# Kernel optimization log

Measured on AMD Instinct MI355X. Metric: run time of the kernel, lower is better.

## Reference

```python
import jax, jax.numpy as jnp
import numpy as np

N_NODES = 4096
F_UAV = 64
N_OBS = N_NODES * F_UAV + 256  # 262400
H = 1024
N_ACT = 64
N_EDGES = 65536


def setup_inputs() -> dict:
    key = jax.random.key(0)
    ks = jax.random.split(key, 13)
    s = lambda fan_in: 1.0 / np.sqrt(fan_in)
    return {
        "node_x": jax.random.normal(ks[0], (N_NODES, F_UAV), jnp.float32),
        "flat_obs": jax.random.normal(ks[1], (N_OBS,), jnp.float32),
        "gcn_w": jax.random.normal(ks[2], (F_UAV, F_UAV), jnp.float32) * s(F_UAV),
        "gcn_b": jnp.zeros((F_UAV,), jnp.float32),
        "w1": jax.random.normal(ks[3], (N_OBS, H), jnp.float32) * s(N_OBS),
        "b1": jnp.zeros((H,), jnp.float32),
        "w2": jax.random.normal(ks[4], (H, H), jnp.float32) * s(H),
        "b2": jnp.zeros((H,), jnp.float32),
        "wv": jax.random.normal(ks[5], (H, 1), jnp.float32) * s(H),
        "bv": jnp.zeros((1,), jnp.float32),
        "wa": jax.random.normal(ks[6], (H, N_ACT), jnp.float32) * s(H),
        "ba": jnp.zeros((N_ACT,), jnp.float32),
        "edge_index": jax.random.randint(ks[7], (2, N_EDGES), 0, N_NODES, jnp.int64),
    }


def _gcn_conv(x, edge_index, w, b):
    n = x.shape[0]
    loops = jnp.arange(n, dtype=edge_index.dtype)
    src = jnp.concatenate([edge_index[0], loops])
    dst = jnp.concatenate([edge_index[1], loops])
    deg = jax.ops.segment_sum(jnp.ones_like(dst, dtype=x.dtype), dst, num_segments=n)
    dinv = jax.lax.rsqrt(deg)  # deg >= 1 thanks to self-loops
    norm = dinv[src] * dinv[dst]          # [E+N]
    h = x @ w                              # [N, F]
    msg = h[src] * norm[:, None]           # gather + scale
    out = jax.ops.segment_sum(msg, dst, num_segments=n)  # scatter-add
    return out + b


def reference(node_x, flat_obs, gcn_w, gcn_b, w1, b1, w2, b2, wv, bv, wa, ba, edge_index):
    y_uav = _gcn_conv(node_x, edge_index, gcn_w, gcn_b).reshape(-1)  # flatten
    x = jnp.concatenate([y_uav, flat_obs[y_uav.shape[0]:]], axis=0)  # [N_OBS]
    y = jax.nn.relu(x @ w1 + b1)
    y = jax.nn.relu(y @ w2 + b2)
    value = y @ wv + bv                    # [1]
    adv = y @ wa + ba                      # [N_ACT]
    return value + adv - jnp.mean(adv, keepdims=True)
```

## Files before the change

kernel.cpp:

```cpp
#include <hip/hip_runtime.h>

#define N_NODES 4096
#define F_UAV 64
#define NOBS 262400
#define GCN_FLAT (N_NODES * F_UAV)
#define HDIM 1024
#define N_ACT 64
#define N_EDGES 65536

typedef float f32x4 __attribute__((ext_vector_type(4)));
typedef float f32x2 __attribute__((ext_vector_type(2)));

#define MV1_GRID 2048
#define MV1_BIGN 256
#define MV1_BIG 129
#define MV1_SMALL 128

#define OFF_X      0
#define OFF_DEG    262400
#define OFF_H      (OFF_DEG + N_NODES)
#define OFF_P1     (OFF_H + GCN_FLAT)
#define OFF_Q1T    (OFF_P1 + 2048*1024)
#define OFF_P2     (OFF_Q1T + 1024*128)

__global__ __launch_bounds__(256) void k_gcn_h(const float* __restrict__ nx,
                                               const float* __restrict__ w,
                                               const int* __restrict__ dst,
                                               float* __restrict__ h,
                                               int* __restrict__ deg) {
    __shared__ float sw[F_UAV * F_UAV];
    __shared__ float sx4[256];
    int tid = threadIdx.x;
    for (int i = tid; i < F_UAV * F_UAV; i += 256) sw[i] = w[i];
    sx4[tid] = nx[blockIdx.x * 256 + tid];
    if (blockIdx.x < 256) atomicAdd(&deg[dst[blockIdx.x * 256 + tid]], 1);
    __syncthreads();
    int r = tid >> 6, j = tid & 63;
    float acc = 0.f;
#pragma unroll
    for (int k = 0; k < F_UAV; ++k) acc += sx4[r * 64 + k] * sw[k * F_UAV + j];
    h[blockIdx.x * 256 + r * 64 + j] = acc;
}

__global__ __launch_bounds__(256) void k_scatter_all(const int* __restrict__ src,
                                                     const int* __restrict__ dst,
                                                     const int* __restrict__ deg,
                                                     const float* __restrict__ h,
                                                     const float* __restrict__ gb,
                                                     const float* __restrict__ obs,
                                                     float* __restrict__ x) {
    int b = blockIdx.x;
    int tid = threadIdx.x;
    if (b < N_EDGES / 4) {
        int e = b * 4 + (tid >> 6);
        int j = tid & 63;
        int s = src[e], d = dst[e];
        float norm = rsqrtf((deg[s] + 1.0f) * (deg[d] + 1.0f));
        atomicAdd(&x[d * 64 + j], h[s * 64 + j] * norm);
    } else if (b < N_EDGES / 4 + 256) {
        int base = (b - N_EDGES / 4) * 1024 + tid * 4;
        int n = base >> 6;
        float dinv2 = 1.0f / (float)(deg[n] + 1);
#pragma unroll
        for (int u = 0; u < 4; ++u) {
            int idx = base + u;
            atomicAdd(&x[idx], h[idx] * dinv2 + gb[idx & 63]);
        }
    } else {
        if (tid < NOBS - GCN_FLAT) x[GCN_FLAT + tid] = obs[GCN_FLAT + tid];
    }
}

__global__ __launch_bounds__(256) void k_matvec(const float* __restrict__ x,
                                                const float* __restrict__ W,
                                                float* __restrict__ part,
                                                int big_n, int big_sz, int small_sz) {
    __shared__ float sx[132];
    int tid = threadIdx.x;
    int b = blockIdx.x;
    int k0 = (b < big_n) ? b * big_sz : big_n * big_sz + (b - big_n) * small_sz;
    int cnt = (b < big_n) ? big_sz : small_sz;
    for (int i = tid; i < cnt; i += 256) sx[i] = x[k0 + i];
    __syncthreads();
    f32x4 acc = {0.f, 0.f, 0.f, 0.f};
    const f32x4* Wr = ((const f32x4*)W) + (size_t)k0 * (HDIM / 4) + tid;
    int kk = cnt & ~7;
    int k = 0;
    for (; k < kk; k += 8) {
#pragma unroll
        for (int u = 0; u < 8; ++u) {
            float xv = sx[k + u];
            f32x4 w = __builtin_nontemporal_load(&Wr[(size_t)(k + u) * (HDIM / 4)]);
            acc += xv * w;
        }
    }
    for (; k < cnt; ++k) acc += sx[k] * __builtin_nontemporal_load(&Wr[(size_t)k * (HDIM / 4)]);
    ((f32x4*)(part + (size_t)b * HDIM))[tid] = acc;
}

template <int NSEG>
__global__ __launch_bounds__(256) void k_sum16T(const float* __restrict__ part,
                                                float* __restrict__ qT) {
    int t = threadIdx.x, s = blockIdx.x;
    const f32x4* p = ((const f32x4*)part) + (size_t)s * 16 * (HDIM / 4) + t;
    f32x4 acc = {0.f, 0.f, 0.f, 0.f};
#pragma unroll
    for (int r = 0; r < 16; ++r) acc += p[(size_t)r * (HDIM / 4)];
#pragma unroll
    for (int u = 0; u < 4; ++u) qT[(size_t)(4 * t + u) * NSEG + s] = acc[u];
}

__global__ __launch_bounds__(256) void k_fin_mv2(const float* __restrict__ q1T,
                                                 const float* __restrict__ b1,
                                                 const float* __restrict__ w2,
                                                 float* __restrict__ p2) {
    __shared__ float s_y[16];
    int t = threadIdx.x, b = blockIdx.x;
    int w = t >> 6, l = t & 63;
#pragma unroll
    for (int rr = 0; rr < 4; ++rr) {
        int j = 16 * b + 4 * w + rr;
        f32x2 v = *(const f32x2*)&q1T[(size_t)j * 128 + 2 * l];
        float sm = v.x + v.y;
        for (int off = 32; off; off >>= 1) sm += __shfl_xor(sm, off);
        if (l == 0) s_y[4 * w + rr] = fmaxf(b1[j] + sm, 0.f);
    }
    __syncthreads();
    f32x4 acc = {0.f, 0.f, 0.f, 0.f};
    const f32x4* Wr = ((const f32x4*)w2) + (size_t)(16 * b) * (HDIM / 4) + t;
#pragma unroll
    for (int i = 0; i < 16; ++i) acc += s_y[i] * Wr[(size_t)i * (HDIM / 4)];
    ((f32x4*)(p2 + (size_t)b * HDIM))[t] = acc;
}

__global__ __launch_bounds__(1024) void k_heads_f(const float* __restrict__ p2,
                                                  const float* __restrict__ b2,
                                                  const float* __restrict__ wv,
                                                  const float* __restrict__ bv,
                                                  const float* __restrict__ wa,
                                                  const float* __restrict__ ba,
                                                  float* __restrict__ out) {
    __shared__ float y2s[1024];
    __shared__ float s_adv[16][64];
    __shared__ float s_pv[1024];
    int t = threadIdx.x;
    float acc = b2[t];
#pragma unroll 8
    for (int s = 0; s < 64; ++s) acc += p2[s * HDIM + t];
    float y = fmaxf(acc, 0.f);
    y2s[t] = y;
    s_pv[t] = y * wv[t];
    __syncthreads();
    int g = t >> 6, a = t & 63;
    float pa = 0.f;
#pragma unroll 4
    for (int kk = 0; kk < 64; ++kk) pa += y2s[g * 64 + kk] * wa[(g * 64 + kk) * 64 + a];
    s_adv[g][a] = pa;
    __syncthreads();
    if (t < 64) {
        float adv = ba[a];
#pragma unroll
        for (int gg = 0; gg < 16; ++gg) adv += s_adv[gg][a];
        float v = 0.f;
#pragma unroll
        for (int i = 0; i < 16; ++i) v += s_pv[a + 64 * i];
        for (int off = 32; off; off >>= 1) v += __shfl_xor(v, off);
        float m = adv;
        for (int off = 32; off; off >>= 1) m += __shfl_xor(m, off);
        m *= (1.f / 64.f);
        out[a] = (v + bv[0]) + adv - m;
    }
}

extern "C" void kernel_launch(void* const* d_in, const int* in_sizes, int n_in,
                              void* d_out, int out_size, void* d_ws, size_t ws_size,
                              hipStream_t stream) {
    const float* node_x   = (const float*)d_in[0];
    const float* flat_obs = (const float*)d_in[1];
    const float* gcn_w    = (const float*)d_in[2];
    const float* gcn_b    = (const float*)d_in[3];
    const float* w1       = (const float*)d_in[4];
    const float* b1       = (const float*)d_in[5];
    const float* w2       = (const float*)d_in[6];
    const float* b2       = (const float*)d_in[7];
    const float* wv       = (const float*)d_in[8];
    const float* bv       = (const float*)d_in[9];
    const float* wa       = (const float*)d_in[10];
    const float* ba       = (const float*)d_in[11];
    const int*   ei       = (const int*)d_in[12];
    const int* src = ei;
    const int* dst = ei + N_EDGES;

    float* ws   = (float*)d_ws;
    float* x    = ws + OFF_X;
    int*   deg  = (int*)(ws + OFF_DEG);
    float* h    = ws + OFF_H;
    float* p1   = ws + OFF_P1;
    float* q1T  = ws + OFF_Q1T;
    float* p2   = ws + OFF_P2;
    float* out  = (float*)d_out;

    hipMemsetAsync(x, 0, (NOBS + N_NODES) * sizeof(float), stream);
    k_gcn_h<<<GCN_FLAT / 256, 256, 0, stream>>>(node_x, gcn_w, dst, h, deg);
    k_scatter_all<<<N_EDGES / 4 + 256 + 1, 256, 0, stream>>>(src, dst, deg, h,
                                                             gcn_b, flat_obs, x);

    k_matvec<<<MV1_GRID, 256, 0, stream>>>(x, w1, p1, MV1_BIGN, MV1_BIG, MV1_SMALL);
    k_sum16T<128><<<128, 256, 0, stream>>>(p1, q1T);
    k_fin_mv2<<<64, 256, 0, stream>>>(q1T, b1, w2, p2);
    k_heads_f<<<1, 1024, 0, stream>>>(p2, b2, wv, bv, wa, ba, out);
}
```

Measured before the change: 231.7 us.

## Replace partial-sum buffers and reduction kernels with atomic accumulation in matvecs

```diff
diff --git a/kernel.cpp b/kernel.cpp
--- a/kernel.cpp
+++ b/kernel.cpp
@@ -9,19 +9,13 @@
 #define N_EDGES 65536
 
 typedef float f32x4 __attribute__((ext_vector_type(4)));
-typedef float f32x2 __attribute__((ext_vector_type(2)));
 
-#define MV1_GRID 2048
-#define MV1_BIGN 256
-#define MV1_BIG 129
-#define MV1_SMALL 128
-
-#define OFF_X      0
-#define OFF_DEG    262400
-#define OFF_H      (OFF_DEG + N_NODES)
-#define OFF_P1     (OFF_H + GCN_FLAT)
-#define OFF_Q1T    (OFF_P1 + 2048*1024)
-#define OFF_P2     (OFF_Q1T + 1024*128)
+#define OFF_X    0
+#define OFF_DEG  NOBS
+#define OFF_Y1A  (OFF_DEG + N_NODES)
+#define OFF_Y2A  (OFF_Y1A + HDIM)
+#define OFF_H    (OFF_Y2A + HDIM)
+#define ZERO_FLOATS (NOBS + N_NODES + 2 * HDIM)
 
 __global__ __launch_bounds__(256) void k_gcn_h(const float* __restrict__ nx,
                                                const float* __restrict__ w,
@@ -71,69 +65,50 @@
     }
 }
 
-__global__ __launch_bounds__(256) void k_matvec(const float* __restrict__ x,
-                                                const float* __restrict__ W,
-                                                float* __restrict__ part,
-                                                int big_n, int big_sz, int small_sz) {
-    __shared__ float sx[132];
-    int tid = threadIdx.x;
-    int b = blockIdx.x;
-    int k0 = (b < big_n) ? b * big_sz : big_n * big_sz + (b - big_n) * small_sz;
-    int cnt = (b < big_n) ? big_sz : small_sz;
-    for (int i = tid; i < cnt; i += 256) sx[i] = x[k0 + i];
+__global__ __launch_bounds__(256) void k_mv1(const float* __restrict__ x,
+                                             const float* __restrict__ W,
+                                             float* __restrict__ y1a) {
+    __shared__ float sx[129];
+    int tid = threadIdx.x, b = blockIdx.x;
+    if (tid < 128) sx[tid] = x[b + 2048 * tid];
+    if (tid == 128) sx[128] = (b < 256) ? x[GCN_FLAT + b] : 0.f;
     __syncthreads();
     f32x4 acc = {0.f, 0.f, 0.f, 0.f};
-    const f32x4* Wr = ((const f32x4*)W) + (size_t)k0 * (HDIM / 4) + tid;
-    int kk = cnt & ~7;
-    int k = 0;
-    for (; k < kk; k += 8) {
-#pragma unroll
-        for (int u = 0; u < 8; ++u) {
-            float xv = sx[k + u];
-            f32x4 w = __builtin_nontemporal_load(&Wr[(size_t)(k + u) * (HDIM / 4)]);
-            acc += xv * w;
-        }
+    const f32x4* p = (const f32x4*)W + (size_t)b * (HDIM / 4) + tid;
+    const size_t stride = (size_t)2048 * (HDIM / 4);
+#pragma unroll 8
+    for (int i = 0; i < 128; ++i)
+        acc += sx[i] * __builtin_nontemporal_load(&p[(size_t)i * stride]);
+    if (b < 256) {
+        const f32x4* pt = (const f32x4*)W + (size_t)(GCN_FLAT + b) * (HDIM / 4) + tid;
+        acc += sx[128] * __builtin_nontemporal_load(pt);
     }
-    for (; k < cnt; ++k) acc += sx[k] * __builtin_nontemporal_load(&Wr[(size_t)k * (HDIM / 4)]);
-    ((f32x4*)(part + (size_t)b * HDIM))[tid] = acc;
+    atomicAdd(&y1a[4 * tid + 0], acc[0]);
+    atomicAdd(&y1a[4 * tid + 1], acc[1]);
+    atomicAdd(&y1a[4 * tid + 2], acc[2]);
+    atomicAdd(&y1a[4 * tid + 3], acc[3]);
 }
 
-template <int NSEG>
-__global__ __launch_bounds__(256) void k_sum16T(const float* __restrict__ part,
-                                                float* __restrict__ qT) {
-    int t = threadIdx.x, s = blockIdx.x;
-    const f32x4* p = ((const f32x4*)part) + (size_t)s * 16 * (HDIM / 4) + t;
+__global__ __launch_bounds__(256) void k_mv2(const float* __restrict__ y1a,
+                                             const float* __restrict__ b1,
+                                             const float* __restrict__ w2,
+                                             float* __restrict__ y2a) {
+    int tid = threadIdx.x, b = blockIdx.x;
+    int j0 = 4 * b;
     f32x4 acc = {0.f, 0.f, 0.f, 0.f};
+    const f32x4* Wr = (const f32x4*)w2 + (size_t)j0 * (HDIM / 4) + tid;
 #pragma unroll
-    for (int r = 0; r < 16; ++r) acc += p[(size_t)r * (HDIM / 4)];
-#pragma unroll
-    for (int u = 0; u < 4; ++u) qT[(size_t)(4 * t + u) * NSEG + s] = acc[u];
+    for (int i = 0; i < 4; ++i) {
+        float y = fmaxf(b1[j0 + i] + y1a[j0 + i], 0.f);
+        acc += y * Wr[(size_t)i * (HDIM / 4)];
+    }
+    atomicAdd(&y2a[4 * tid + 0], acc[0]);
+    atomicAdd(&y2a[4 * tid + 1], acc[1]);
+    atomicAdd(&y2a[4 * tid + 2], acc[2]);
+    atomicAdd(&y2a[4 * tid + 3], acc[3]);
 }
 
-__global__ __launch_bounds__(256) void k_fin_mv2(const float* __restrict__ q1T,
-                                                 const float* __restrict__ b1,
-                                                 const float* __restrict__ w2,
-                                                 float* __restrict__ p2) {
-    __shared__ float s_y[16];
-    int t = threadIdx.x, b = blockIdx.x;
-    int w = t >> 6, l = t & 63;
-#pragma unroll
-    for (int rr = 0; rr < 4; ++rr) {
-        int j = 16 * b + 4 * w + rr;
-        f32x2 v = *(const f32x2*)&q1T[(size_t)j * 128 + 2 * l];
-        float sm = v.x + v.y;
-        for (int off = 32; off; off >>= 1) sm += __shfl_xor(sm, off);
-        if (l == 0) s_y[4 * w + rr] = fmaxf(b1[j] + sm, 0.f);
-    }
-    __syncthreads();
-    f32x4 acc = {0.f, 0.f, 0.f, 0.f};
-    const f32x4* Wr = ((const f32x4*)w2) + (size_t)(16 * b) * (HDIM / 4) + t;
-#pragma unroll
-    for (int i = 0; i < 16; ++i) acc += s_y[i] * Wr[(size_t)i * (HDIM / 4)];
-    ((f32x4*)(p2 + (size_t)b * HDIM))[t] = acc;
-}
-
-__global__ __launch_bounds__(1024) void k_heads_f(const float* __restrict__ p2,
+__global__ __launch_bounds__(1024) void k_heads_f(const float* __restrict__ y2a,
                                                   const float* __restrict__ b2,
                                                   const float* __restrict__ wv,
                                                   const float* __restrict__ bv,
@@ -144,10 +119,7 @@
     __shared__ float s_adv[16][64];
     __shared__ float s_pv[1024];
     int t = threadIdx.x;
-    float acc = b2[t];
-#pragma unroll 8
-    for (int s = 0; s < 64; ++s) acc += p2[s * HDIM + t];
-    float y = fmaxf(acc, 0.f);
+    float y = fmaxf(b2[t] + y2a[t], 0.f);
     y2s[t] = y;
     s_pv[t] = y * wv[t];
     __syncthreads();
@@ -194,19 +166,17 @@
     float* ws   = (float*)d_ws;
     float* x    = ws + OFF_X;
     int*   deg  = (int*)(ws + OFF_DEG);
+    float* y1a  = ws + OFF_Y1A;
+    float* y2a  = ws + OFF_Y2A;
     float* h    = ws + OFF_H;
-    float* p1   = ws + OFF_P1;
-    float* q1T  = ws + OFF_Q1T;
-    float* p2   = ws + OFF_P2;
     float* out  = (float*)d_out;
 
-    hipMemsetAsync(x, 0, (NOBS + N_NODES) * sizeof(float), stream);
+    hipMemsetAsync(x, 0, ZERO_FLOATS * sizeof(float), stream);
     k_gcn_h<<<GCN_FLAT / 256, 256, 0, stream>>>(node_x, gcn_w, dst, h, deg);
     k_scatter_all<<<N_EDGES / 4 + 256 + 1, 256, 0, stream>>>(src, dst, deg, h,
                                                              gcn_b, flat_obs, x);
 
-    k_matvec<<<MV1_GRID, 256, 0, stream>>>(x, w1, p1, MV1_BIGN, MV1_BIG, MV1_SMALL);
-    k_sum16T<128><<<128, 256, 0, stream>>>(p1, q1T);
-    k_fin_mv2<<<64, 256, 0, stream>>>(q1T, b1, w2, p2);
-    k_heads_f<<<1, 1024, 0, stream>>>(p2, b2, wv, bv, wa, ba, out);
+    k_mv1<<<2048, 256, 0, stream>>>(x, w1, y1a);
+    k_mv2<<<256, 256, 0, stream>>>(y1a, b1, w2, y2a);
+    k_heads_f<<<1, 1024, 0, stream>>>(y2a, b2, wv, bv, wa, ba, out);
 }
```

After: 338.0 us. +45.9%, slower.
